# Performance work log

Hardware: AMD Instinct MI355X
Metric: run time of the kernel (lower is better)

Reference implementation:

```python
import jax, jax.numpy as jnp
import numpy as np

N, E, D, C, NEG_SLOPE = 50000, 800000, 128, 40, 0.2


def setup_inputs() -> dict:
    key = jax.random.key(0)
    ks = jax.random.split(key, 20)
    inp = {
        'x': jax.random.normal(ks[0], (N, D), dtype=jnp.float32),
        'edge_index': jax.random.randint(ks[1], (2, E), 0, N, dtype=jnp.int64),
    }
    s = 1.0 / np.sqrt(D)
    for l in range(3):
        inp[f'W{l}'] = jax.random.normal(ks[2 + 4 * l], (D, D), dtype=jnp.float32) * s
        inp[f'a_src{l}'] = jax.random.normal(ks[3 + 4 * l], (D,), dtype=jnp.float32) * s
        inp[f'a_dst{l}'] = jax.random.normal(ks[4 + 4 * l], (D,), dtype=jnp.float32) * s
        inp[f'b{l}'] = jnp.zeros((D,), dtype=jnp.float32)
    inp['W_head'] = jax.random.normal(ks[14], (D, C), dtype=jnp.float32) * s
    inp['b_head'] = jnp.zeros((C,), dtype=jnp.float32)
    return inp


def gat_layer(x, src, dst, W, a_src, a_dst, b):
    # x: [N, D]; src/dst: [E+N] (self-loops included)
    h = x @ W                                   # [N, D] node transform
    e_s = h @ a_src                             # [N] source attention logits
    e_d = h @ a_dst                             # [N] dest attention logits
    alpha = jax.nn.leaky_relu(e_s[src] + e_d[dst], NEG_SLOPE)  # [E+N]
    # segment softmax over incoming edges of each dst node
    m = jax.ops.segment_max(alpha, dst, num_segments=N)
    ex = jnp.exp(alpha - m[dst])
    z = jax.ops.segment_sum(ex, dst, num_segments=N)
    w = ex / z[dst]                             # [E+N] normalized attention
    out = jax.ops.segment_sum(w[:, None] * h[src], dst, num_segments=N)
    return out + b


def reference(x, edge_index, W0, a_src0, a_dst0, b0, W1, a_src1, a_dst1, b1,
              W2, a_src2, a_dst2, b2, W_head, b_head):
    loops = jnp.arange(N, dtype=edge_index.dtype)
    src = jnp.concatenate([edge_index[0], loops])  # PyG add_self_loops=True
    dst = jnp.concatenate([edge_index[1], loops])
    for W, a_s, a_d, b in ((W0, a_src0, a_dst0, b0),
                           (W1, a_src1, a_dst1, b1),
                           (W2, a_src2, a_dst2, b2)):
        x = jax.nn.relu(gat_layer(x, src, dst, W, a_s, a_d, b))
        # dropout is identity in eval mode
    return x @ W_head + b_head
```

## Files before the change

### kernel.cpp

```cpp
#include <hip/hip_runtime.h>
#include <hip/hip_bf16.h>

#define NN 50000
#define EE 800000
#define DD 128
#define CC 40
#define NEG 0.2f
#define NPAD 50048
#define NB 782
#define CEDGES 2048
#define NSCAT 391
#define PADCAP 2048
#define DEGCAP 64
#define XSTR 136

typedef _Float16 half8 __attribute__((ext_vector_type(8)));
typedef unsigned short ushort8 __attribute__((ext_vector_type(8)));
typedef float floatx4 __attribute__((ext_vector_type(4)));

__device__ __forceinline__ float lrelu(float a) { return a > 0.f ? a : NEG * a; }
__device__ __forceinline__ float bf2f(unsigned short u) {
    union { unsigned int i; float f; } v; v.i = (unsigned int)u << 16; return v.f;
}

__device__ __forceinline__ int edge_at(const void* ei, int i64, long long idx) {
    return i64 ? (int)((const long long*)ei)[idx] : ((const int*)ei)[idx];
}

struct ParamCvt {
    const void* src[11];
    int off[11];
    int total;
};

__global__ __launch_bounds__(256) void prep_kernel(ParamCvt a,
                                                   const void* __restrict__ x_raw,
                                                   const void* __restrict__ ei,
                                                   const void* __restrict__ W0,
                                                   const void* __restrict__ W1,
                                                   const void* __restrict__ W2,
                                                   const void* __restrict__ Wh,
                                                   int* __restrict__ flags,
                                                   int* __restrict__ cursor,
                                                   unsigned int* __restrict__ pairs,
                                                   float* __restrict__ params,
                                                   _Float16* __restrict__ wpack) {
    __shared__ int cnt[NB];
    __shared__ int loff[NB];
    __shared__ int gbase[NB];
    __shared__ unsigned int lp[CEDGES];
    __shared__ int wsum[4];
    __shared__ int carry;
    int t = threadIdx.x, lane = t & 63, wid = t >> 6;
    if (blockIdx.x < NSCAT) {
        unsigned int hi0 = ((const unsigned int*)ei)[2 * lane + 1];
        int i64 = (__ballot(hi0 != 0u) == 0ull) ? 1 : 0;
        for (int i = t; i < NB; i += 256) cnt[i] = 0;
        if (t == 0) carry = 0;
        __syncthreads();
        int base = blockIdx.x * CEDGES;
        int sreg[8], dreg[8];
        #pragma unroll
        for (int j = 0; j < 8; ++j) {
            int e = base + j * 256 + t;
            if (e < EE) {
                sreg[j] = edge_at(ei, i64, e);
                dreg[j] = edge_at(ei, i64, (long long)EE + e);
                atomicAdd(&cnt[dreg[j] >> 6], 1);
            } else { sreg[j] = -1; dreg[j] = -1; }
        }
        __syncthreads();
        for (int c0 = 0; c0 < NB; c0 += 256) {
            int i = c0 + t;
            int v = (i < NB) ? cnt[i] : 0;
            int x = v;
            #pragma unroll
            for (int o = 1; o < 64; o <<= 1) {
                int y = __shfl_up(x, o, 64);
                if (lane >= o) x += y;
            }
            if (lane == 63) wsum[wid] = x;
            __syncthreads();
            int carr = carry;
            int woff = 0;
            for (int w = 0; w < wid; ++w) woff += wsum[w];
            if (i < NB) loff[i] = carr + woff + x - v;
            __syncthreads();
            if (t == 0) carry = carr + wsum[0] + wsum[1] + wsum[2] + wsum[3];
            __syncthreads();
        }
        for (int i = t; i < NB; i += 256) {
            int c = cnt[i];
            gbase[i] = c ? atomicAdd(&cursor[i], c) : 0;
        }
        __syncthreads();
        for (int i = t; i < NB; i += 256) cnt[i] = loff[i];
        __syncthreads();
        #pragma unroll
        for (int j = 0; j < 8; ++j) {
            if (dreg[j] >= 0) {
                int slot = atomicAdd(&cnt[dreg[j] >> 6], 1);
                lp[slot] = ((unsigned int)dreg[j] << 16) | (unsigned int)sreg[j];
            }
        }
        __syncthreads();
        int total = (EE - base < CEDGES) ? (EE - base) : CEDGES;
        for (int i = t; i < total; i += 256) {
            unsigned int pr = lp[i];
            int b = (int)(pr >> 22);
            int idx = gbase[b] + (i - loff[b]);
            if (idx < PADCAP)
                __builtin_nontemporal_store(pr, &pairs[(size_t)b * PADCAP + idx]);
        }
        return;
    }
    int cb = blockIdx.x - NSCAT;
    unsigned short u = ((const unsigned short*)x_raw)[lane * 2];
    int e = (u >> 7) & 0xFF;
    int bad = (!(e >= 96 && e <= 158) && u != 0 && u != 0x8000) ? 1 : 0;
    int bf = (__ballot(bad) == 0ull) ? 1 : 0;
    if (cb == 265) {
        unsigned int hi = ((const unsigned int*)ei)[2 * lane + 1];
        int i64 = (__ballot(hi != 0u) == 0ull) ? 1 : 0;
        if (t == 0) { flags[0] = bf; flags[1] = i64; }
        return;
    }
    if (cb < 192) {
        int i = cb * 256 + t;
        int l = i >> 14, r = i & 16383;
        int j = r & 7, ln = (r >> 3) & 63, ks = (r >> 9) & 3, c = r >> 11;
        int k = ks * 32 + (ln >> 4) * 8 + j;
        int ncol = c * 16 + (ln & 15);
        const void* W = (l == 0) ? W0 : ((l == 1) ? W1 : W2);
        float v = bf ? bf2f(((const unsigned short*)W)[k * 128 + ncol])
                     : ((const float*)W)[k * 128 + ncol];
        wpack[i] = (_Float16)v;
    } else if (cb < 240) {
        int i = (cb - 192) * 256 + t;
        int p = (i >= 6144) ? 1 : 0;
        int r = i - p * 6144;
        int j = r & 7, ln = (r >> 3) & 63, ks = (r >> 9) & 3, c = r >> 11;
        int k = ks * 32 + (ln >> 4) * 8 + j;
        int ncol = c * 16 + (ln & 15);
        float wv = 0.f;
        if (ncol < CC)
            wv = bf ? bf2f(((const unsigned short*)Wh)[k * CC + ncol])
                    : ((const float*)Wh)[k * CC + ncol];
        _Float16 hi = (_Float16)wv;
        wpack[3 * 16384 + i] = p ? (_Float16)(wv - (float)hi) : hi;
    } else {
        int i = (cb - 240) * 256 + t;
        if (i >= a.total) return;
        int k = 0;
        #pragma unroll
        for (int j = 1; j < 11; ++j) if (i >= a.off[j]) k = j;
        int local = i - a.off[k];
        params[i] = bf ? bf2f(((const unsigned short*)a.src[k])[local])
                       : ((const float*)a.src[k])[local];
    }
}

__device__ __forceinline__ void gemm_core(const half8 a[4], const _Float16* __restrict__ Wg,
                                          const float* __restrict__ asrc,
                                          const float* __restrict__ adst,
                                          _Float16* __restrict__ H,
                                          float* __restrict__ es, float* __restrict__ ed,
                                          int n, int rowbase, int lane) {
    int quad = lane >> 4, col = lane & 15;
    float esp[4] = {0, 0, 0, 0}, edp[4] = {0, 0, 0, 0};
    #pragma unroll
    for (int c = 0; c < 8; ++c) {
        floatx4 acc = {0.f, 0.f, 0.f, 0.f};
        #pragma unroll
        for (int ks = 0; ks < 4; ++ks) {
            half8 b = *(const half8*)&Wg[(((c * 4 + ks) * 64) + lane) * 8];
            acc = __builtin_amdgcn_mfma_f32_16x16x32_f16(a[ks], b, acc, 0, 0, 0);
        }
        float av = asrc[c * 16 + col], dv = adst[c * 16 + col];
        #pragma unroll
        for (int r = 0; r < 4; ++r) {
            int rowg = rowbase + quad * 4 + r;
            if (rowg < n) H[(size_t)rowg * 128 + c * 16 + col] = (_Float16)acc[r];
            esp[r] += acc[r] * av;
            edp[r] += acc[r] * dv;
        }
    }
    #pragma unroll
    for (int r = 0; r < 4; ++r) {
        float s = esp[r], d = edp[r];
        #pragma unroll
        for (int o = 1; o < 16; o <<= 1) {
            s += __shfl_xor(s, o, 64);
            d += __shfl_xor(d, o, 64);
        }
        int rowg = rowbase + quad * 4 + r;
        if (col == 0 && rowg < n) { es[rowg] = s; ed[rowg] = d; }
    }
}

__device__ __forceinline__ void agg_body(const _Float16* __restrict__ H,
                                         const int* __restrict__ cnt,
                                         const unsigned short* __restrict__ csr,
                                         const float* __restrict__ es,
                                         const float* __restrict__ ed,
                                         const float* __restrict__ bias,
                                         _Float16* __restrict__ xt,
                                         int n, int blk32, int t) {
    int sub = t & 15, g = t >> 4;
    int f0 = sub * 8;
    #pragma unroll 1
    for (int r = 0; r < 2; ++r) {
        int node = blk32 + r * 16 + g;
        if (node >= n) continue;
        int total = cnt[node];
        size_t beg = (size_t)node << 6;
        float edi = ed[node];
        float wself = __expf(lrelu(es[node] + edi));
        float z = wself;
        half8 hs = *(const half8*)&H[(size_t)node * 128 + f0];
        float acc[8];
        #pragma unroll
        for (int j = 0; j < 8; ++j) acc[j] = wself * (float)hs[j];
        ushort8 c8n = *(const ushort8*)&csr[beg];
        for (int base = 0; base < total; base += 8) {
            ushort8 c8 = c8n;
            c8n = *(const ushort8*)&csr[beg + ((base + 8) & 63)];
            int sdx[8];
            #pragma unroll
            for (int d = 0; d < 8; ++d)
                sdx[d] = (base + d < total) ? (int)c8[d] : node;
            half8 h[8];
            #pragma unroll
            for (int d = 0; d < 8; ++d)
                h[d] = *(const half8*)&H[(size_t)sdx[d] * 128 + f0];
            float wd[8];
            #pragma unroll
            for (int d = 0; d < 8; ++d) {
                float ee = __expf(lrelu(es[sdx[d]] + edi));
                wd[d] = (base + d < total) ? ee : 0.f;
                z += wd[d];
            }
            #pragma unroll
            for (int d = 0; d < 8; ++d) {
                #pragma unroll
                for (int j = 0; j < 8; ++j) acc[j] += wd[d] * (float)h[d][j];
            }
        }
        float invz = 1.f / z;
        half8 o8;
        #pragma unroll
        for (int j = 0; j < 8; ++j)
            o8[j] = (_Float16)fmaxf(acc[j] * invz + bias[f0 + j], 0.f);
        *(half8*)&xt[(size_t)(r * 16 + g) * XSTR + f0] = o8;
    }
}

__global__ __launch_bounds__(256) void bucketD_gemm0(const unsigned int* __restrict__ pairs,
                                                     const int* __restrict__ cursor,
                                                     int* __restrict__ cnt,
                                                     unsigned short* __restrict__ csr,
                                                     const void* __restrict__ Xraw,
                                                     const int* __restrict__ flags,
                                                     const _Float16* __restrict__ Wp,
                                                     const float* __restrict__ asrc,
                                                     const float* __restrict__ adst,
                                                     _Float16* __restrict__ H,
                                                     float* __restrict__ es,
                                                     float* __restrict__ ed, int n) {
    __shared__ unsigned short lcsr[4096];
    __shared__ int curS[64];
    int t = threadIdx.x;
    if (blockIdx.x < NB) {
        if (t < 64) curS[t] = 0;
        __syncthreads();
        int b = blockIdx.x;
        int cntb = cursor[b];
        if (cntb > PADCAP) cntb = PADCAP;
        int pbeg = b * PADCAP;
        for (int i = t; i < cntb; i += 256) {
            unsigned int pr = pairs[pbeg + i];
            int nd = (pr >> 16) & 63;
            int p = atomicAdd(&curS[nd], 1);
            if (p < DEGCAP) lcsr[nd * 64 + p] = (unsigned short)(pr & 0xFFFF);
        }
        __syncthreads();
        if (t < 64) {
            int gid = b * 64 + t;
            if (gid < NN) {
                int v = curS[t];
                cnt[gid] = v > DEGCAP ? DEGCAP : v;
            }
        }
        for (int i = t; i < 512; i += 256)
            __builtin_nontemporal_store(((const ushort8*)lcsr)[i],
                                        &((ushort8*)csr)[(size_t)b * 512 + i]);
        return;
    }
    int gb = blockIdx.x - NB;
    int w = t >> 6, lane = t & 63;
    int quad = lane >> 4, col = lane & 15;
    int rowbase = gb * 64 + w * 16;
    half8 a[4];
    int bf = flags[0];
    int row = rowbase + col;
    if (row >= n) row = n - 1;
    if (bf) {
        const unsigned short* xr = (const unsigned short*)Xraw + (size_t)row * 128 + quad * 8;
        #pragma unroll
        for (int ks = 0; ks < 4; ++ks) {
            ushort8 u = *(const ushort8*)(xr + ks * 32);
            #pragma unroll
            for (int j = 0; j < 8; ++j) a[ks][j] = (_Float16)bf2f(u[j]);
        }
    } else {
        const float* xr = (const float*)Xraw + (size_t)row * 128 + quad * 8;
        #pragma unroll
        for (int ks = 0; ks < 4; ++ks) {
            float4 f0 = *(const float4*)(xr + ks * 32);
            float4 f1 = *(const float4*)(xr + ks * 32 + 4);
            a[ks][0] = (_Float16)f0.x; a[ks][1] = (_Float16)f0.y;
            a[ks][2] = (_Float16)f0.z; a[ks][3] = (_Float16)f0.w;
            a[ks][4] = (_Float16)f1.x; a[ks][5] = (_Float16)f1.y;
            a[ks][6] = (_Float16)f1.z; a[ks][7] = (_Float16)f1.w;
        }
    }
    gemm_core(a, Wp, asrc, adst, H, es, ed, n, rowbase, lane);
}

__global__ __launch_bounds__(256) void fused_ag(const _Float16* __restrict__ Hin,
                                                const int* __restrict__ cnt,
                                                const unsigned short* __restrict__ csr,
                                                const float* __restrict__ esin,
                                                const float* __restrict__ edin,
                                                const float* __restrict__ bias,
                                                const _Float16* __restrict__ Wp,
                                                const float* __restrict__ asrc,
                                                const float* __restrict__ adst,
                                                _Float16* __restrict__ Hout,
                                                float* __restrict__ esout,
                                                float* __restrict__ edout, int n) {
    __shared__ _Float16 xt[32 * XSTR];
    int t = threadIdx.x;
    agg_body(Hin, cnt, csr, esin, edin, bias, xt, n, blockIdx.x * 32, t);
    __syncthreads();
    int w = t >> 6, lane = t & 63;
    if (w >= 2) return;
    int quad = lane >> 4, col = lane & 15;
    int rowbase = blockIdx.x * 32 + w * 16;
    int rl = w * 16 + col;
    half8 a[4];
    #pragma unroll
    for (int ks = 0; ks < 4; ++ks)
        a[ks] = *(const half8*)&xt[(size_t)rl * XSTR + ks * 32 + quad * 8];
    gemm_core(a, Wp, asrc, adst, Hout, esout, edout, n, rowbase, lane);
}

__global__ __launch_bounds__(256) void fused_ah(const _Float16* __restrict__ Hin,
                                                const int* __restrict__ cnt,
                                                const unsigned short* __restrict__ csr,
                                                const float* __restrict__ esin,
                                                const float* __restrict__ edin,
                                                const float* __restrict__ bias,
                                                const _Float16* __restrict__ WhP,
                                                const float* __restrict__ bhf,
                                                const int* __restrict__ flags,
                                                void* __restrict__ out, int n) {
    __shared__ _Float16 xt[32 * XSTR];
    int t = threadIdx.x;
    agg_body(Hin, cnt, csr, esin, edin, bias, xt, n, blockIdx.x * 32, t);
    __syncthreads();
    int w = t >> 6, lane = t & 63;
    if (w >= 2) return;
    int quad = lane >> 4, col = lane & 15;
    int rowbase = blockIdx.x * 32 + w * 16;
    int rl = w * 16 + col;
    half8 a[4];
    #pragma unroll
    for (int ks = 0; ks < 4; ++ks)
        a[ks] = *(const half8*)&xt[(size_t)rl * XSTR + ks * 32 + quad * 8];
    int bf = flags[0];
    #pragma unroll
    for (int c = 0; c < 3; ++c) {
        floatx4 acc = {0.f, 0.f, 0.f, 0.f};
        #pragma unroll
        for (int ks = 0; ks < 4; ++ks) {
            half8 b = *(const half8*)&WhP[(((c * 4 + ks) * 64) + lane) * 8];
            acc = __builtin_amdgcn_mfma_f32_16x16x32_f16(a[ks], b, acc, 0, 0, 0);
        }
        #pragma unroll
        for (int ks = 0; ks < 4; ++ks) {
            half8 b = *(const half8*)&WhP[6144 + (((c * 4 + ks) * 64) + lane) * 8];
            acc = __builtin_amdgcn_mfma_f32_16x16x32_f16(a[ks], b, acc, 0, 0, 0);
        }
        int ocol = c * 16 + col;
        if (ocol < CC) {
            float bv = bhf[ocol];
            if (bf) {
                __hip_bfloat16* ob = (__hip_bfloat16*)out;
                #pragma unroll
                for (int r = 0; r < 4; ++r) {
                    int rowg = rowbase + quad * 4 + r;
                    if (rowg < n) ob[(size_t)rowg * CC + ocol] = __float2bfloat16(acc[r] + bv);
                }
            } else {
                float* of = (float*)out;
                #pragma unroll
                for (int r = 0; r < 4; ++r) {
                    int rowg = rowbase + quad * 4 + r;
                    if (rowg < n) of[(size_t)rowg * CC + ocol] = acc[r] + bv;
                }
            }
        }
    }
}

extern "C" void kernel_launch(void* const* d_in, const int* in_sizes, int n_in,
                              void* d_out, int out_size, void* d_ws, size_t ws_size,
                              hipStream_t stream) {
    const void* x_raw = d_in[0];
    const void* ei    = d_in[1];

    char* p = (char*)d_ws;
    auto alloc = [&](size_t bytes) { void* r = (void*)p; p += (bytes + 255) & ~(size_t)255; return r; };
    int*            flags  = (int*)alloc(16);
    _Float16*       H0     = (_Float16*)alloc((size_t)NPAD * DD * 2);
    _Float16*       H1     = (_Float16*)alloc((size_t)NPAD * DD * 2);
    float*          es0    = (float*)alloc((size_t)NN * 4);
    float*          ed0    = (float*)alloc((size_t)NN * 4);
    float*          es1    = (float*)alloc((size_t)NN * 4);
    float*          ed1    = (float*)alloc((size_t)NN * 4);
    int*            cnt    = (int*)alloc((size_t)NN * 4);
    unsigned short* csr    = (unsigned short*)alloc((size_t)NB * 4096 * 2);
    unsigned int*   pairs  = (unsigned int*)alloc((size_t)NB * PADCAP * 4);
    int*            cursor = (int*)alloc((size_t)NB * 4);
    _Float16*       wpack  = (_Float16*)alloc((size_t)(3 * 16384 + 12288) * 2);
    float*          params = (float*)alloc((size_t)(3 * 384 + 5160) * 4);

    ParamCvt pc;
    {
        int k = 0, off = 0;
        auto add = [&](const void* s, int nel) { pc.src[k] = s; pc.off[k] = off; off += nel; ++k; };
        for (int l = 0; l < 3; ++l) {
            add(d_in[3 + 4 * l], 128);
            add(d_in[4 + 4 * l], 128);
            add(d_in[5 + 4 * l], 128);
        }
        add(d_in[14], 5120);
        add(d_in[15], 40);
        pc.total = off;
    }

    hipMemsetAsync(cursor, 0, (size_t)NB * 4, stream);
    prep_kernel<<<NSCAT + 266, 256, 0, stream>>>(pc, x_raw, ei, d_in[2], d_in[6], d_in[10],
                                                 d_in[14], flags, cursor, pairs, params, wpack);

    const int ngb64 = NPAD / 64;
    const int ngb32 = NPAD / 32;
    float* base0 = params;
    float* base1 = params + 384;
    float* base2 = params + 768;
    _Float16* whpack = wpack + 3 * 16384;
    bucketD_gemm0<<<NB + ngb64, 256, 0, stream>>>(pairs, cursor, cnt, csr,
                                                  x_raw, flags, wpack, base0, base0 + 128,
                                                  H0, es0, ed0, NN);
    fused_ag<<<ngb32, 256, 0, stream>>>(H0, cnt, csr, es0, ed0, base0 + 256,
                                        wpack + 16384, base1, base1 + 128,
                                        H1, es1, ed1, NN);
    fused_ag<<<ngb32, 256, 0, stream>>>(H1, cnt, csr, es1, ed1, base1 + 256,
                                        wpack + 32768, base2, base2 + 128,
                                        H0, es0, ed0, NN);
    fused_ah<<<ngb32, 256, 0, stream>>>(H0, cnt, csr, es0, ed0, base2 + 256,
                                        whpack, params + 1152 + 5120, flags, d_out, NN);
}
```

Measured before the change: 259.6 us.

## Precompute edge attention weights once per block into LDS before aggregation

Before, each of the 16 feature-slice threads of a node recomputed exp(leaky_relu(es[src]+ed[dst])) for every neighbour. The new code adds a pass where 8 threads per node compute those weights once and store them in shared memory, and the aggregation loop then reads them from LDS. This removes redundant es gathers and exp evaluations. The CSR scratch is now zero-initialised so padded slots hold valid indices, which drops the per-edge select, and launch bounds request 3 blocks per SM. The cost is an extra 8KB of shared memory per block and one more barrier.

```diff
diff --git a/kernel.cpp b/kernel.cpp
--- a/kernel.cpp
+++ b/kernel.cpp
@@ -17,6 +17,7 @@
 typedef _Float16 half8 __attribute__((ext_vector_type(8)));
 typedef unsigned short ushort8 __attribute__((ext_vector_type(8)));
 typedef float floatx4 __attribute__((ext_vector_type(4)));
+typedef float float8 __attribute__((ext_vector_type(8)));
 
 __device__ __forceinline__ float lrelu(float a) { return a > 0.f ? a : NEG * a; }
 __device__ __forceinline__ float bf2f(unsigned short u) {
@@ -198,61 +199,72 @@
     }
 }
 
-__device__ __forceinline__ void agg_body(const _Float16* __restrict__ H,
+__device__ __forceinline__ void wpass_block(const int* __restrict__ cnt,
+                                            const unsigned short* __restrict__ csr,
+                                            const float* __restrict__ es,
+                                            const float* __restrict__ ed,
+                                            float* __restrict__ wlds,
+                                            int n, int blk32, int t) {
+    int nloc = t >> 3, cb8 = (t & 7) << 3;
+    int node = blk32 + nloc;
+    float8 wv = {0.f, 0.f, 0.f, 0.f, 0.f, 0.f, 0.f, 0.f};
+    if (node < n) {
+        int total = cnt[node];
+        if (cb8 < total) {
+            ushort8 c8 = *(const ushort8*)&csr[((size_t)node << 6) + cb8];
+            float edi = ed[node];
+            #pragma unroll
+            for (int d = 0; d < 8; ++d) {
+                float e = __expf(lrelu(es[(int)c8[d]] + edi));
+                wv[d] = (cb8 + d < total) ? e : 0.f;
+            }
+        }
+    }
+    *(float8*)&wlds[nloc * 64 + cb8] = wv;
+}
+
+__device__ __forceinline__ void agg_node(const _Float16* __restrict__ H,
                                          const int* __restrict__ cnt,
                                          const unsigned short* __restrict__ csr,
                                          const float* __restrict__ es,
                                          const float* __restrict__ ed,
                                          const float* __restrict__ bias,
+                                         const float* __restrict__ wrow,
                                          _Float16* __restrict__ xt,
-                                         int n, int blk32, int t) {
-    int sub = t & 15, g = t >> 4;
-    int f0 = sub * 8;
-    #pragma unroll 1
-    for (int r = 0; r < 2; ++r) {
-        int node = blk32 + r * 16 + g;
-        if (node >= n) continue;
-        int total = cnt[node];
-        size_t beg = (size_t)node << 6;
-        float edi = ed[node];
-        float wself = __expf(lrelu(es[node] + edi));
-        float z = wself;
-        half8 hs = *(const half8*)&H[(size_t)node * 128 + f0];
-        float acc[8];
-        #pragma unroll
-        for (int j = 0; j < 8; ++j) acc[j] = wself * (float)hs[j];
-        ushort8 c8n = *(const ushort8*)&csr[beg];
-        for (int base = 0; base < total; base += 8) {
-            ushort8 c8 = c8n;
-            c8n = *(const ushort8*)&csr[beg + ((base + 8) & 63)];
-            int sdx[8];
+                                         int n, int node, int lrow, int f0) {
+    if (node >= n) return;
+    int total = cnt[node];
+    size_t beg = (size_t)node << 6;
+    float edi = ed[node];
+    float wself = __expf(lrelu(es[node] + edi));
+    float z = wself;
+    half8 hs = *(const half8*)&H[(size_t)node * 128 + f0];
+    float acc[8];
+    #pragma unroll
+    for (int j = 0; j < 8; ++j) acc[j] = wself * (float)hs[j];
+    ushort8 c8n = *(const ushort8*)&csr[beg];
+    for (int base = 0; base < total; base += 8) {
+        ushort8 c8 = c8n;
+        c8n = *(const ushort8*)&csr[beg + ((base + 8) & 63)];
+        float8 wd = *(const float8*)&wrow[base];
+        half8 h[8];
+        #pragma unroll
+        for (int d = 0; d < 8; ++d)
+            h[d] = *(const half8*)&H[(size_t)(int)c8[d] * 128 + f0];
+        #pragma unroll
+        for (int d = 0; d < 8; ++d) z += wd[d];
+        #pragma unroll
+        for (int d = 0; d < 8; ++d) {
             #pragma unroll
-            for (int d = 0; d < 8; ++d)
-                sdx[d] = (base + d < total) ? (int)c8[d] : node;
-            half8 h[8];
-            #pragma unroll
-            for (int d = 0; d < 8; ++d)
-                h[d] = *(const half8*)&H[(size_t)sdx[d] * 128 + f0];
-            float wd[8];
-            #pragma unroll
-            for (int d = 0; d < 8; ++d) {
-                float ee = __expf(lrelu(es[sdx[d]] + edi));
-                wd[d] = (base + d < total) ? ee : 0.f;
-                z += wd[d];
-            }
-            #pragma unroll
-            for (int d = 0; d < 8; ++d) {
-                #pragma unroll
-                for (int j = 0; j < 8; ++j) acc[j] += wd[d] * (float)h[d][j];
-            }
-        }
-        float invz = 1.f / z;
-        half8 o8;
-        #pragma unroll
-        for (int j = 0; j < 8; ++j)
-            o8[j] = (_Float16)fmaxf(acc[j] * invz + bias[f0 + j], 0.f);
-        *(half8*)&xt[(size_t)(r * 16 + g) * XSTR + f0] = o8;
-    }
+            for (int j = 0; j < 8; ++j) acc[j] += wd[d] * (float)h[d][j];
+        }
+    }
+    float invz = 1.f / z;
+    half8 o8;
+    #pragma unroll
+    for (int j = 0; j < 8; ++j)
+        o8[j] = (_Float16)fmaxf(acc[j] * invz + bias[f0 + j], 0.f);
+    *(half8*)&xt[(size_t)lrow * XSTR + f0] = o8;
 }
 
 __global__ __launch_bounds__(256) void bucketD_gemm0(const unsigned int* __restrict__ pairs,
@@ -271,6 +283,7 @@
     __shared__ int curS[64];
     int t = threadIdx.x;
     if (blockIdx.x < NB) {
+        for (int i = t; i < 4096; i += 256) lcsr[i] = 0;
         if (t < 64) curS[t] = 0;
         __syncthreads();
         int b = blockIdx.x;
@@ -327,26 +340,35 @@
     gemm_core(a, Wp, asrc, adst, H, es, ed, n, rowbase, lane);
 }
 
-__global__ __launch_bounds__(256) void fused_ag(const _Float16* __restrict__ Hin,
-                                                const int* __restrict__ cnt,
-                                                const unsigned short* __restrict__ csr,
-                                                const float* __restrict__ esin,
-                                                const float* __restrict__ edin,
-                                                const float* __restrict__ bias,
-                                                const _Float16* __restrict__ Wp,
-                                                const float* __restrict__ asrc,
-                                                const float* __restrict__ adst,
-                                                _Float16* __restrict__ Hout,
-                                                float* __restrict__ esout,
-                                                float* __restrict__ edout, int n) {
+__global__ __launch_bounds__(256, 3) void fused_ag(const _Float16* __restrict__ Hin,
+                                                   const int* __restrict__ cnt,
+                                                   const unsigned short* __restrict__ csr,
+                                                   const float* __restrict__ esin,
+                                                   const float* __restrict__ edin,
+                                                   const float* __restrict__ bias,
+                                                   const _Float16* __restrict__ Wp,
+                                                   const float* __restrict__ asrc,
+                                                   const float* __restrict__ adst,
+                                                   _Float16* __restrict__ Hout,
+                                                   float* __restrict__ esout,
+                                                   float* __restrict__ edout, int n) {
     __shared__ _Float16 xt[32 * XSTR];
+    __shared__ float wlds[32 * 64];
     int t = threadIdx.x;
-    agg_body(Hin, cnt, csr, esin, edin, bias, xt, n, blockIdx.x * 32, t);
+    int blk32 = blockIdx.x * 32;
+    wpass_block(cnt, csr, esin, edin, wlds, n, blk32, t);
+    __syncthreads();
+    int sub = t & 15, g = t >> 4;
+    int f0 = sub * 8;
+    #pragma unroll 1
+    for (int r = 0; r < 2; ++r)
+        agg_node(Hin, cnt, csr, esin, edin, bias, &wlds[(r * 16 + g) * 64], xt,
+                 n, blk32 + r * 16 + g, r * 16 + g, f0);
     __syncthreads();
     int w = t >> 6, lane = t & 63;
     if (w >= 2) return;
     int quad = lane >> 4, col = lane & 15;
-    int rowbase = blockIdx.x * 32 + w * 16;
+    int rowbase = blk32 + w * 16;
     int rl = w * 16 + col;
     half8 a[4];
     #pragma unroll
@@ -355,24 +377,33 @@
     gemm_core(a, Wp, asrc, adst, Hout, esout, edout, n, rowbase, lane);
 }
 
-__global__ __launch_bounds__(256) void fused_ah(const _Float16* __restrict__ Hin,
-                                                const int* __restrict__ cnt,
-                                                const unsigned short* __restrict__ csr,
-                                                const float* __restrict__ esin,
-                                                const float* __restrict__ edin,
-                                                const float* __restrict__ bias,
-                                                const _Float16* __restrict__ WhP,
-                                                const float* __restrict__ bhf,
-                                                const int* __restrict__ flags,
-                                                void* __restrict__ out, int n) {
+__global__ __launch_bounds__(256, 3) void fused_ah(const _Float16* __restrict__ Hin,
+                                                   const int* __restrict__ cnt,
+                                                   const unsigned short* __restrict__ csr,
+                                                   const float* __restrict__ esin,
+                                                   const float* __restrict__ edin,
+                                                   const float* __restrict__ bias,
+                                                   const _Float16* __restrict__ WhP,
+                                                   const float* __restrict__ bhf,
+                                                   const int* __restrict__ flags,
+                                                   void* __restrict__ out, int n) {
     __shared__ _Float16 xt[32 * XSTR];
+    __shared__ float wlds[32 * 64];
     int t = threadIdx.x;
-    agg_body(Hin, cnt, csr, esin, edin, bias, xt, n, blockIdx.x * 32, t);
+    int blk32 = blockIdx.x * 32;
+    wpass_block(cnt, csr, esin, edin, wlds, n, blk32, t);
+    __syncthreads();
+    int sub = t & 15, g = t >> 4;
+    int f0 = sub * 8;
+    #pragma unroll 1
+    for (int r = 0; r < 2; ++r)
+        agg_node(Hin, cnt, csr, esin, edin, bias, &wlds[(r * 16 + g) * 64], xt,
+                 n, blk32 + r * 16 + g, r * 16 + g, f0);
     __syncthreads();
     int w = t >> 6, lane = t & 63;
     if (w >= 2) return;
     int quad = lane >> 4, col = lane & 15;
-    int rowbase = blockIdx.x * 32 + w * 16;
+    int rowbase = blk32 + w * 16;
     int rl = w * 16 + col;
     half8 a[4];
     #pragma unroll
```

Result: no change. 257.0 us (-1.0%).
